# Kernel optimization log

Hardware: AMD Instinct MI355X
Metric: run time of the kernel (lower is better)

The kernel has to match this reference:

```python
import jax, jax.numpy as jnp
import numpy as np

B, N, D, H, L = 16, 1024, 256, 128, 2  # batch, nodes, feat dim, gcn_hidden, n_layers (D == 2*H)


def setup_inputs() -> dict:
    key = jax.random.key(0)
    ks = jax.random.split(key, 16)
    inp = {
        "gcn_input": jax.random.normal(ks[0], (B, N, D), jnp.float32),
        # scale adjacencies by 1/N so aggregated features stay O(1)
        "latent_adj": jax.random.uniform(ks[1], (B, N, N), jnp.float32) / N,
        "dep_adj": jax.random.uniform(ks[2], (B, N, N), jnp.float32) / N,
        # stacked per-layer parameters (leading dim L); layers share shapes since D == 2*H
        "refine_gate": jax.random.normal(ks[3], (L, D, 1), jnp.float32) * 0.02,
        "gate_W_in": jax.random.normal(ks[4], (L, D, 1), jnp.float32) * 0.02,
        "gate_b_in": jnp.zeros((L, 1), jnp.float32),
        "gate_W_out": jax.random.normal(ks[5], (L, D, 1), jnp.float32) * 0.02,
        "gate_b_out": jnp.zeros((L, 1), jnp.float32),
        "fc_in_W": jax.random.normal(ks[6], (L, H, D), jnp.float32) * 0.02,
        "fc_in_b": jnp.zeros((L, H), jnp.float32),
        "fc_out_W": jax.random.normal(ks[7], (L, H, D), jnp.float32) * 0.02,
        "fc_out_b": jnp.zeros((L, H), jnp.float32),
        "ln_g": jnp.ones((L, 2 * H), jnp.float32),
        "ln_b": jnp.zeros((L, 2 * H), jnp.float32),
    }
    return inp


def _gcn_layer(x, latent, dep, rg, Wgi, bgi, Wgo, bgo, Wi, bi, Wo, bo, g, b):
    # refine gate blends dependency and latent adjacency per source node
    gate = jax.nn.sigmoid(x @ rg)  # [B,N,1]
    A_in = gate * dep + (1.0 - gate) * latent  # [B,N,N]
    A_out = gate * jnp.swapaxes(dep, -1, -2) + (1.0 - gate) * jnp.swapaxes(latent, -1, -2)
    Ax_in = A_in @ x   # [B,N,D]
    Ax_out = A_out @ x
    # gcn gates (scalar bias added after the gated product, as in torch)
    Ax_in = Ax_in * jax.nn.sigmoid(Ax_in @ Wgi) + bgi
    Ax_out = Ax_out * jax.nn.sigmoid(Ax_out @ Wgo) + bgo
    # rec_fc(Ax) + rec_fc(x): weight applied to sum, bias counted twice (faithful)
    h_in = (Ax_in + x) @ Wi.T + 2.0 * bi   # [B,N,H]
    h_out = (Ax_out + x) @ Wo.T + 2.0 * bo
    h = jnp.concatenate([h_in, h_out], axis=-1)  # [B,N,2H]
    mu = jnp.mean(h, axis=-1, keepdims=True)
    var = jnp.var(h, axis=-1, keepdims=True)
    h = (h - mu) * jax.lax.rsqrt(var + 1e-5) * g + b
    return jax.nn.gelu(h, approximate=False)


def reference(gcn_input, latent_adj, dep_adj, refine_gate, gate_W_in, gate_b_in,
              gate_W_out, gate_b_out, fc_in_W, fc_in_b, fc_out_W, fc_out_b, ln_g, ln_b):
    x = gcn_input
    for l in range(refine_gate.shape[0]):  # small fixed layer count
        x = _gcn_layer(x, latent_adj, dep_adj, refine_gate[l],
                       gate_W_in[l], gate_b_in[l], gate_W_out[l], gate_b_out[l],
                       fc_in_W[l], fc_in_b[l], fc_out_W[l], fc_out_b[l],
                       ln_g[l], ln_b[l])
    return x
```

## Files before the change

### kernel.cpp

```cpp
#include <hip/hip_runtime.h>
#include <hip/hip_bf16.h>
#include <cstdint>

#define B_ 16
#define N_ 1024
#define D_ 256
#define H_ 128

typedef unsigned short u16;
typedef __attribute__((ext_vector_type(8))) short bf16x8;
typedef __attribute__((ext_vector_type(4))) float f32x4;

__device__ __forceinline__ u16 f2bf(float f) {
    union { float f; uint32_t u; } v; v.f = f;
    return (u16)((v.u + 0x7FFFu + ((v.u >> 16) & 1u)) >> 16);
}
__device__ __forceinline__ float bf2f(u16 h) {
    union { uint32_t u; float f; } v; v.u = ((uint32_t)h) << 16;
    return v.f;
}

typedef __attribute__((address_space(3))) void lds_void;
typedef const __attribute__((address_space(1))) void g_void;

__device__ __forceinline__ void gl_lds16(const void* g, void* l) {
    __builtin_amdgcn_global_load_lds((g_void*)g, (lds_void*)l, 16, 0, 0);
}

__device__ __forceinline__ void vm_wait4() { asm volatile("s_waitcnt vmcnt(4)" ::: "memory"); }
__device__ __forceinline__ void vm_wait3() { asm volatile("s_waitcnt vmcnt(3)" ::: "memory"); }
__device__ __forceinline__ void vm_wait2() { asm volatile("s_waitcnt vmcnt(2)" ::: "memory"); }
__device__ __forceinline__ void vm_wait0() { asm volatile("s_waitcnt vmcnt(0)" ::: "memory"); }
__device__ __forceinline__ void lgkm0()   { asm volatile("s_waitcnt lgkmcnt(0)" ::: "memory"); }
__device__ __forceinline__ void schedb()  { __builtin_amdgcn_sched_barrier(0); }

__global__ __launch_bounds__(256) void k_conv_adj(
    const float* __restrict__ dep, const float* __restrict__ lat,
    u16* __restrict__ depb, u16* __restrict__ latb,
    u16* __restrict__ depTb, u16* __restrict__ latTb)
{
    __shared__ u16 tile[64][64];
    const int bz = blockIdx.z;
    const int b = bz >> 1;
    const float* src = (bz & 1) ? lat : dep;
    u16* dstN = (bz & 1) ? latb : depb;
    u16* dstT = (bz & 1) ? latTb : depTb;
    const int r0 = blockIdx.y * 64, c0 = blockIdx.x * 64;
    const int t = threadIdx.x;
    const int r = t >> 2, cg = (t & 3) * 16;

    const float* srow = src + ((size_t)b * N_ + r0 + r) * N_ + c0 + cg;
    bf16x8 lo, hi;
    {
        const float4 v0 = *(const float4*)(srow);
        const float4 v1 = *(const float4*)(srow + 4);
        const float4 v2 = *(const float4*)(srow + 8);
        const float4 v3 = *(const float4*)(srow + 12);
        lo[0] = (short)f2bf(v0.x); lo[1] = (short)f2bf(v0.y); lo[2] = (short)f2bf(v0.z); lo[3] = (short)f2bf(v0.w);
        lo[4] = (short)f2bf(v1.x); lo[5] = (short)f2bf(v1.y); lo[6] = (short)f2bf(v1.z); lo[7] = (short)f2bf(v1.w);
        hi[0] = (short)f2bf(v2.x); hi[1] = (short)f2bf(v2.y); hi[2] = (short)f2bf(v2.z); hi[3] = (short)f2bf(v2.w);
        hi[4] = (short)f2bf(v3.x); hi[5] = (short)f2bf(v3.y); hi[6] = (short)f2bf(v3.z); hi[7] = (short)f2bf(v3.w);
    }
    u16* nrow = dstN + ((size_t)b * N_ + r0 + r) * N_ + c0 + cg;
    *(bf16x8*)nrow = lo;
    *(bf16x8*)(nrow + 8) = hi;

    const int g0 = (t & 3) * 2;
    const int s = (r & 7) ^ ((r >> 3) & 7);
    *(bf16x8*)(&tile[r][((g0    ) ^ s) * 8]) = lo;
    *(bf16x8*)(&tile[r][((g0 + 1) ^ s) * 8]) = hi;
    __syncthreads();

    const int sc = t >> 2, rg2 = (t & 3) * 16;
    bf16x8 o0, o1;
    #pragma unroll
    for (int i = 0; i < 8; ++i) {
        const int R = rg2 + i;
        const int sR = (R & 7) ^ ((R >> 3) & 7);
        o0[i] = (short)tile[R][(((sc >> 3) ^ sR) * 8) + (sc & 7)];
    }
    #pragma unroll
    for (int i = 0; i < 8; ++i) {
        const int R = rg2 + 8 + i;
        const int sR = (R & 7) ^ ((R >> 3) & 7);
        o1[i] = (short)tile[R][(((sc >> 3) ^ sR) * 8) + (sc & 7)];
    }
    u16* dT = dstT + ((size_t)b * N_ + c0 + sc) * N_ + r0 + rg2;
    *(bf16x8*)dT = o0;
    *(bf16x8*)(dT + 8) = o1;
}

__global__ __launch_bounds__(256) void k_gate_xt(
    const float* __restrict__ x, const float* __restrict__ rg,
    float* __restrict__ gate, u16* __restrict__ xT,
    const float* __restrict__ wi, const float* __restrict__ wo,
    u16* __restrict__ wib, u16* __restrict__ wob)
{
    if (blockIdx.y >= B_) {
        const int i = ((blockIdx.y - B_) * 32 + blockIdx.x) * 256 + threadIdx.x;
        wib[i] = f2bf(wi[i]);
        wob[i] = f2bf(wo[i]);
        return;
    }

    __shared__ u16 lx[D_][36];
    __shared__ float srg[D_];
    const int b = blockIdx.y, n0 = blockIdx.x * 32;
    const int t = threadIdx.x;
    srg[t] = rg[t];
    __syncthreads();

    const int r = t >> 3, cg = t & 7;
    const float* xrow = x + ((size_t)b * N_ + n0 + r) * D_;
    float dot = 0.f;
    #pragma unroll
    for (int u = 0; u < 8; ++u) {
        const int c = cg * 32 + u * 4;
        const float4 v = *(const float4*)(xrow + c);
        lx[c][r] = f2bf(v.x); lx[c + 1][r] = f2bf(v.y);
        lx[c + 2][r] = f2bf(v.z); lx[c + 3][r] = f2bf(v.w);
        dot += v.x * srg[c] + v.y * srg[c + 1] + v.z * srg[c + 2] + v.w * srg[c + 3];
    }
    dot += __shfl_down(dot, 4, 8);
    dot += __shfl_down(dot, 2, 8);
    dot += __shfl_down(dot, 1, 8);
    if (cg == 0) gate[(size_t)b * N_ + n0 + r] = 1.f / (1.f + expf(-dot));
    __syncthreads();

    #pragma unroll
    for (int i = 0; i < 8; ++i) {
        const int unit = i * 256 + t;
        const int d = unit >> 3, nch = (unit & 7) * 4;
        ushort4 wv;
        wv.x = lx[d][nch];     wv.y = lx[d][nch + 1];
        wv.z = lx[d][nch + 2]; wv.w = lx[d][nch + 3];
        *(ushort4*)(xT + ((size_t)b * D_ + d) * N_ + n0 + nch) = wv;
    }
}

__global__ __launch_bounds__(512, 2) void k_gemm_ax(
    const u16* __restrict__ depb, const u16* __restrict__ latb,
    const u16* __restrict__ depTb, const u16* __restrict__ latTb,
    const u16* __restrict__ xT,
    const float* __restrict__ gate,
    const float* __restrict__ Wgi, const float* __restrict__ Wgo,
    const float* __restrict__ bgi, const float* __restrict__ bgo,
    const float* __restrict__ xcur,
    u16* __restrict__ axin, u16* __restrict__ axout)
{
    __shared__ __align__(16) char smem[51712];
    u16* const sb = (u16*)smem;
    float* hbuf = (float*)smem;
    float* psum = (float*)(smem + 49152);
    float* sh_s = (float*)(smem + 51200);

    const int bid = blockIdx.x;
    const int logical = (bid & 7) * 32 + (bid >> 3);
    const int b = logical >> 4;
    const int rem = logical & 15;
    const int z = rem >> 3;
    const int m0 = (rem & 7) * 128;

    const u16* A1 = z ? depTb : depb;
    const u16* A2 = z ? latTb : latb;
    const float* Wg = z ? Wgo : Wgi;
    const float bg0 = z ? bgo[0] : bgi[0];
    u16* outp = z ? axout : axin;

    const int t = threadIdx.x;
    const int lane = t & 63;
    const int w = t >> 6;
    const int wr = w >> 2, wc = w & 3;

    const int arow = t >> 2;
    const int akq = t & 3;
    const float gv = gate[(size_t)b * N_ + m0 + arow];
    const u16* gA1 = A1 + ((size_t)b * N_ + m0 + arow) * N_ + akq * 8;
    const u16* gA2 = A2 + ((size_t)b * N_ + m0 + arow) * N_ + akq * 8;
    const int awoff = arow * 32 + ((akq ^ ((arow >> 1) & 3)) << 3);

    const int rl = lane >> 2;
    const int kk = (((lane & 3) ^ ((lane >> 3) & 3)) << 3);
    const u16* gB0 = xT + ((size_t)b * D_ + (w * 2) * 16 + rl) * N_ + kk;
    const u16* gB1 = xT + ((size_t)b * D_ + (w * 2 + 1) * 16 + rl) * N_ + kk;
    const int boff0 = 4096 + (w * 2) * 512;
    const int boff1 = 4096 + (w * 2 + 1) * 512;

    const int mrow = lane & 15;
    const int hi = lane >> 4;
    const int kg = (((lane >> 4) ^ ((mrow >> 1) & 3)) << 3);

    f32x4 acc[4][4];
    const f32x4 fz = {0.f, 0.f, 0.f, 0.f};
    #pragma unroll
    for (int i = 0; i < 4; ++i)
        #pragma unroll
        for (int j = 0; j < 4; ++j) acc[i][j] = fz;

    bf16x8 rA1x, rA2x, rA1y, rA2y;

    auto blend_store = [&](const bf16x8& a1v, const bf16x8& a2v, u16* dst) {
        bf16x8 bl;
        #pragma unroll
        for (int u = 0; u < 8; ++u) {
            const float f1 = bf2f((u16)a1v[u]);
            const float f2 = bf2f((u16)a2v[u]);
            bl[u] = (short)f2bf(f2 + gv * (f1 - f2));
        }
        *(bf16x8*)dst = bl;
    };

    rA1x = *(const bf16x8*)(gA1);       rA2x = *(const bf16x8*)(gA2);
    blend_store(rA1x, rA2x, sb + awoff);
    rA1x = *(const bf16x8*)(gA1 + 32);  rA2x = *(const bf16x8*)(gA2 + 32);
    gl_lds16(gB0, sb + boff0);          gl_lds16(gB1, sb + boff1);
    blend_store(rA1x, rA2x, sb + 12288 + awoff);
    rA1x = *(const bf16x8*)(gA1 + 64);  rA2x = *(const bf16x8*)(gA2 + 64);
    gl_lds16(gB0 + 32, sb + 12288 + boff0); gl_lds16(gB1 + 32, sb + 12288 + boff1);
    vm_wait2();
    lgkm0();
    schedb(); __builtin_amdgcn_s_barrier(); schedb();

    auto body = [&](int ks, bf16x8& c1, bf16x8& c2, bf16x8& n1, bf16x8& n2) {
        if (ks <= 28) {
            n1 = *(const bf16x8*)(gA1 + (ks + 3) * 32);
            n2 = *(const bf16x8*)(gA2 + (ks + 3) * 32);
        }
        const u16* sA = sb + (ks & 1) * 12288;
        const u16* sBc = sA + 4096;
        bf16x8 a[4], fbv[4];
        #pragma unroll
        for (int mt = 0; mt < 4; ++mt)
            a[mt] = *(const bf16x8*)(sA + (wr * 64 + mt * 16 + mrow) * 32 + kg);
        #pragma unroll
        for (int nt = 0; nt < 4; ++nt)
            fbv[nt] = *(const bf16x8*)(sBc + (wc * 64 + nt * 16 + mrow) * 32 + kg);
        #pragma unroll
        for (int mt = 0; mt < 4; ++mt)
            #pragma unroll
            for (int nt = 0; nt < 4; ++nt)
                acc[mt][nt] = __builtin_amdgcn_mfma_f32_16x16x32_bf16(a[mt], fbv[nt], acc[mt][nt], 0, 0, 0);
        schedb();
        __builtin_amdgcn_s_barrier();
        schedb();
        if (ks <= 29) {
            u16* cb = sb + (ks & 1) * 12288;
            blend_store(c1, c2, cb + awoff);
            gl_lds16(gB0 + (ks + 2) * 32, cb + boff0);
            gl_lds16(gB1 + (ks + 2) * 32, cb + boff1);
        }
        if (ks <= 28) vm_wait4();
        else if (ks == 29) vm_wait2();
        else if (ks == 30) vm_wait0();
        lgkm0();
        schedb();
        __builtin_amdgcn_s_barrier();
        schedb();
    };

    for (int kp = 0; kp < 16; ++kp) {
        body(2 * kp,     rA1x, rA2x, rA1y, rA2y);
        body(2 * kp + 1, rA1y, rA2y, rA1x, rA2x);
    }
    __syncthreads();

    float wgv[4];
    #pragma unroll
    for (int nt = 0; nt < 4; ++nt) wgv[nt] = Wg[wc * 64 + nt * 16 + mrow];
    #pragma unroll
    for (int mt = 0; mt < 4; ++mt) {
        #pragma unroll
        for (int rr = 0; rr < 4; ++rr) {
            float p = acc[mt][0][rr] * wgv[0] + acc[mt][1][rr] * wgv[1]
                    + acc[mt][2][rr] * wgv[2] + acc[mt][3][rr] * wgv[3];
            p += __shfl_xor(p, 1, 16);
            p += __shfl_xor(p, 2, 16);
            p += __shfl_xor(p, 4, 16);
            p += __shfl_xor(p, 8, 16);
            if (mrow == 0) psum[(wr * 64 + mt * 16 + hi * 4 + rr) * 4 + wc] = p;
        }
    }
    __syncthreads();
    if (t < 128) {
        const float d = psum[t * 4] + psum[t * 4 + 1] + psum[t * 4 + 2] + psum[t * 4 + 3];
        sh_s[t] = 1.f / (1.f + expf(-d));
    }
    __syncthreads();

    #pragma unroll
    for (int p = 0; p < 4; ++p) {
        if (wr == (p >> 1)) {
            #pragma unroll
            for (int mtl = 0; mtl < 2; ++mtl) {
                const int mt = (p & 1) * 2 + mtl;
                #pragma unroll
                for (int nt = 0; nt < 4; ++nt) {
                    const int col = wc * 64 + nt * 16 + mrow;
                    #pragma unroll
                    for (int rr = 0; rr < 4; ++rr) {
                        const int hrow = mtl * 16 + hi * 4 + rr;
                        hbuf[hrow * 260 + col] = acc[mt][nt][rr];
                    }
                }
            }
        }
        __syncthreads();
        {
            const int sr = t >> 4;
            const int sc0 = (t & 15) * 16;
            const int grow = p * 32 + sr;
            const float s = sh_s[grow];
            const size_t gb = ((size_t)b * N_ + m0 + grow) * D_ + sc0;
            const float* xr = xcur + gb;
            u16* orow = outp + gb;
            bf16x8 o0, o1;
            #pragma unroll
            for (int u = 0; u < 8; ++u)
                o0[u] = (short)f2bf(hbuf[sr * 260 + sc0 + u] * s + bg0 + xr[u]);
            #pragma unroll
            for (int u = 0; u < 8; ++u)
                o1[u] = (short)f2bf(hbuf[sr * 260 + sc0 + 8 + u] * s + bg0 + xr[8 + u]);
            *(bf16x8*)orow = o0;
            *(bf16x8*)(orow + 8) = o1;
        }
        __syncthreads();
    }
}

template<int FUSE>
__global__ __launch_bounds__(512, 2) void k_fc_ln(
    const u16* __restrict__ axin, const u16* __restrict__ axout,
    const u16* __restrict__ Wib, const u16* __restrict__ Wob,
    const float* __restrict__ bi, const float* __restrict__ bo,
    const float* __restrict__ lg, const float* __restrict__ lb,
    float* __restrict__ outp,
    const float* __restrict__ rgN, float* __restrict__ gateN,
    u16* __restrict__ xTN)
{
    __shared__ __align__(16) char smem[51712];
    u16* const sb = (u16*)smem;
    float* hbuf = (float*)smem;
    float* psum = (float*)(smem + 49152);
    float* sh_mu = (float*)(smem + 51200);
    float* sh_rs = (float*)(smem + 51456);

    const int bid = blockIdx.x;
    const int logical = (bid & 7) * 32 + (bid >> 3);
    const int b = logical >> 4;
    const int m0 = (logical & 15) * 64;

    const int t = threadIdx.x, lane = t & 63, w = t >> 6;
    const int wr = w >> 2, wc = w & 3;
    const int half = wc >> 1;

    const int rl = lane >> 2;
    const int kk = (((lane & 3) ^ ((lane >> 3) & 3)) << 3);

    const u16* gsrc[3];
    int loff[3];
    #pragma unroll
    for (int ci = 0; ci < 3; ++ci) {
        const int c = w * 3 + ci;
        if (c < 4) {
            gsrc[ci] = axin + ((size_t)b * N_ + m0 + c * 16 + rl) * D_ + kk;
            loff[ci] = c * 512;
        } else if (c < 8) {
            gsrc[ci] = axout + ((size_t)b * N_ + m0 + (c - 4) * 16 + rl) * D_ + kk;
            loff[ci] = 2048 + (c - 4) * 512;
        } else {
            const int cw = c - 8;
            const u16* base = (cw < 8) ? (Wib + (size_t)(cw * 16 + rl) * D_)
                                       : (Wob + (size_t)((cw - 8) * 16 + rl) * D_);
            gsrc[ci] = base + kk;
            loff[ci] = 4096 + cw * 512;
        }
    }

    f32x4 acc[2][4];
    const f32x4 fz = {0.f, 0.f, 0.f, 0.f};
    #pragma unroll
    for (int i = 0; i < 2; ++i)
        #pragma unroll
        for (int j = 0; j < 4; ++j) acc[i][j] = fz;

    #pragma unroll
    for (int ci = 0; ci < 3; ++ci) gl_lds16(gsrc[ci], sb + loff[ci]);
    #pragma unroll
    for (int ci = 0; ci < 3; ++ci) gl_lds16(gsrc[ci] + 32, sb + 12288 + loff[ci]);
    vm_wait3();
    lgkm0();
    schedb(); __builtin_amdgcn_s_barrier(); schedb();

    const int mrow = lane & 15;
    const int hi = lane >> 4;
    const int kg = (((lane >> 4) ^ ((mrow >> 1) & 3)) << 3);

    for (int ks = 0; ks < 8; ++ks) {
        const u16* cur = sb + (ks & 1) * 12288;
        const u16* sA = cur + (half ? 2048 : 0);
        const u16* sW = cur + 4096;
        bf16x8 a[2], fbv[4];
        #pragma unroll
        for (int mt = 0; mt < 2; ++mt)
            a[mt] = *(const bf16x8*)(sA + (wr * 32 + mt * 16 + mrow) * 32 + kg);
        #pragma unroll
        for (int nt = 0; nt < 4; ++nt)
            fbv[nt] = *(const bf16x8*)(sW + (wc * 64 + nt * 16 + mrow) * 32 + kg);
        #pragma unroll
        for (int mt = 0; mt < 2; ++mt)
            #pragma unroll
            for (int nt = 0; nt < 4; ++nt)
                acc[mt][nt] = __builtin_amdgcn_mfma_f32_16x16x32_bf16(a[mt], fbv[nt], acc[mt][nt], 0, 0, 0);
        schedb();
        __builtin_amdgcn_s_barrier();
        schedb();
        if (ks <= 5) {
            u16* nb = sb + (ks & 1) * 12288;
            #pragma unroll
            for (int ci = 0; ci < 3; ++ci) gl_lds16(gsrc[ci] + (ks + 2) * 32, nb + loff[ci]);
        }
        if (ks <= 5) vm_wait3();
        else if (ks == 6) vm_wait0();
        lgkm0();
        schedb();
        __builtin_amdgcn_s_barrier();
        schedb();
    }
    __syncthreads();

    float bc[4];
    #pragma unroll
    for (int nt = 0; nt < 4; ++nt) {
        const int colh = wc * 64 + nt * 16 + mrow;
        bc[nt] = 2.f * (colh < 128 ? bi[colh] : bo[colh - 128]);
    }
    #pragma unroll
    for (int mt = 0; mt < 2; ++mt)
        #pragma unroll
        for (int rr = 0; rr < 4; ++rr) {
            const int lrow = wr * 32 + mt * 16 + hi * 4 + rr;
            float s = 0.f, ss = 0.f;
            #pragma unroll
            for (int nt = 0; nt < 4; ++nt) {
                const float v = acc[mt][nt][rr] + bc[nt];
                s += v; ss += v * v;
            }
            s += __shfl_xor(s, 1, 16);  ss += __shfl_xor(ss, 1, 16);
            s += __shfl_xor(s, 2, 16);  ss += __shfl_xor(ss, 2, 16);
            s += __shfl_xor(s, 4, 16);  ss += __shfl_xor(ss, 4, 16);
            s += __shfl_xor(s, 8, 16);  ss += __shfl_xor(ss, 8, 16);
            if (mrow == 0) {
                psum[lrow * 8 + wc * 2] = s;
                psum[lrow * 8 + wc * 2 + 1] = ss;
            }
        }
    __syncthreads();
    if (t < 64) {
        const float s = psum[t * 8] + psum[t * 8 + 2] + psum[t * 8 + 4] + psum[t * 8 + 6];
        const float ss = psum[t * 8 + 1] + psum[t * 8 + 3] + psum[t * 8 + 5] + psum[t * 8 + 7];
        const float mu = s * (1.f / 256.f);
        const float var = ss * (1.f / 256.f) - mu * mu;
        sh_mu[t] = mu;
        sh_rs[t] = rsqrtf(var + 1e-5f);
    }
    __syncthreads();

    #pragma unroll
    for (int p = 0; p < 2; ++p) {
        if (wr == p) {
            #pragma unroll
            for (int mt = 0; mt < 2; ++mt)
                #pragma unroll
                for (int nt = 0; nt < 4; ++nt) {
                    const int col = wc * 64 + nt * 16 + mrow;
                    #pragma unroll
                    for (int rr = 0; rr < 4; ++rr) {
                        const int hrow = mt * 16 + hi * 4 + rr;
                        hbuf[hrow * 260 + col] = acc[mt][nt][rr] + bc[nt];
                    }
                }
        }
        __syncthreads();
        {
            const int sr = t >> 4;
            const int sc0 = (t & 15) * 16;
            const int grow = p * 32 + sr;
            const float mu = sh_mu[grow], rs = sh_rs[grow];
            float* orow = outp + ((size_t)b * N_ + m0 + grow) * D_ + sc0;
            float gdot = 0.f;
            #pragma unroll
            for (int q = 0; q < 4; ++q) {
                const float4 gg = *(const float4*)(lg + sc0 + q * 4);
                const float4 bb = *(const float4*)(lb + sc0 + q * 4);
                float4 o;
                const float v0 = (hbuf[sr * 260 + sc0 + q * 4    ] - mu) * rs * gg.x + bb.x;
                const float v1 = (hbuf[sr * 260 + sc0 + q * 4 + 1] - mu) * rs * gg.y + bb.y;
                const float v2 = (hbuf[sr * 260 + sc0 + q * 4 + 2] - mu) * rs * gg.z + bb.z;
                const float v3 = (hbuf[sr * 260 + sc0 + q * 4 + 3] - mu) * rs * gg.w + bb.w;
                o.x = 0.5f * v0 * (1.f + erff(v0 * 0.70710678118654752f));
                o.y = 0.5f * v1 * (1.f + erff(v1 * 0.70710678118654752f));
                o.z = 0.5f * v2 * (1.f + erff(v2 * 0.70710678118654752f));
                o.w = 0.5f * v3 * (1.f + erff(v3 * 0.70710678118654752f));
                *(float4*)(orow + q * 4) = o;
                if (FUSE) {
                    hbuf[sr * 260 + sc0 + q * 4    ] = o.x;
                    hbuf[sr * 260 + sc0 + q * 4 + 1] = o.y;
                    hbuf[sr * 260 + sc0 + q * 4 + 2] = o.z;
                    hbuf[sr * 260 + sc0 + q * 4 + 3] = o.w;
                    const float4 rv = *(const float4*)(rgN + sc0 + q * 4);
                    gdot += o.x * rv.x + o.y * rv.y + o.z * rv.z + o.w * rv.w;
                }
            }
            if (FUSE) {
                gdot += __shfl_xor(gdot, 1, 16);
                gdot += __shfl_xor(gdot, 2, 16);
                gdot += __shfl_xor(gdot, 4, 16);
                gdot += __shfl_xor(gdot, 8, 16);
                if ((t & 15) == 0)
                    gateN[(size_t)b * N_ + m0 + grow] = 1.f / (1.f + expf(-gdot));
            }
        }
        __syncthreads();
        if (FUSE) {
            const int d = t >> 1;
            const int nh = (t & 1) * 16;
            bf16x8 y0, y1;
            #pragma unroll
            for (int i = 0; i < 8; ++i)
                y0[i] = (short)f2bf(hbuf[(nh + i) * 260 + d]);
            #pragma unroll
            for (int i = 0; i < 8; ++i)
                y1[i] = (short)f2bf(hbuf[(nh + 8 + i) * 260 + d]);
            u16* xrow = xTN + ((size_t)b * D_ + d) * N_ + m0 + p * 32 + nh;
            *(bf16x8*)xrow = y0;
            *(bf16x8*)(xrow + 8) = y1;
            __syncthreads();
        }
    }
}

extern "C" void kernel_launch(void* const* d_in, const int* in_sizes, int n_in,
                              void* d_out, int out_size, void* d_ws, size_t ws_size,
                              hipStream_t stream)
{
    (void)in_sizes; (void)n_in; (void)out_size; (void)ws_size;

    const float* x0  = (const float*)d_in[0];
    const float* lat = (const float*)d_in[1];
    const float* dep = (const float*)d_in[2];
    const float* rg  = (const float*)d_in[3];
    const float* Wgi = (const float*)d_in[4];
    const float* bgi = (const float*)d_in[5];
    const float* Wgo = (const float*)d_in[6];
    const float* bgo = (const float*)d_in[7];
    const float* fiW = (const float*)d_in[8];
    const float* fib = (const float*)d_in[9];
    const float* foW = (const float*)d_in[10];
    const float* fob = (const float*)d_in[11];
    const float* lng = (const float*)d_in[12];
    const float* lnb = (const float*)d_in[13];

    char* ws = (char*)d_ws;
    size_t off = 0;
    auto alloc = [&](size_t bytes) {
        char* p = ws + off;
        off += (bytes + 255) & ~(size_t)255;
        return p;
    };
    u16* depb  = (u16*)alloc(2ull * B_ * N_ * N_);
    u16* latb  = (u16*)alloc(2ull * B_ * N_ * N_);
    u16* depTb = (u16*)alloc(2ull * B_ * N_ * N_);
    u16* latTb = (u16*)alloc(2ull * B_ * N_ * N_);
    u16* xT    = (u16*)alloc(2ull * B_ * D_ * N_);
    u16* axin  = (u16*)alloc(2ull * B_ * N_ * D_);
    u16* axout = (u16*)alloc(2ull * B_ * N_ * D_);
    float* gate = (float*)alloc(4ull * B_ * N_);
    float* xbuf = (float*)alloc(4ull * B_ * N_ * D_);
    u16* Wib = (u16*)alloc(2ull * 2 * H_ * D_);
    u16* Wob = (u16*)alloc(2ull * 2 * H_ * D_);

    k_conv_adj<<<dim3(16, 16, 32), 256, 0, stream>>>(dep, lat, depb, latb, depTb, latTb);

    k_gate_xt<<<dim3(32, B_ + 8), 256, 0, stream>>>(
        x0, rg, gate, xT, fiW, foW, Wib, Wob);

    k_gemm_ax<<<dim3(256), 512, 0, stream>>>(
        depb, latb, depTb, latTb, xT, gate,
        Wgi, Wgo, bgi, bgo, x0, axin, axout);
    k_fc_ln<1><<<dim3(256), 512, 0, stream>>>(
        axin, axout, Wib, Wob, fib, fob, lng, lnb,
        xbuf, rg + D_, gate, xT);

    k_gemm_ax<<<dim3(256), 512, 0, stream>>>(
        depb, latb, depTb, latTb, xT, gate,
        Wgi + D_, Wgo + D_, bgi + 1, bgo + 1, xbuf, axin, axout);
    k_fc_ln<0><<<dim3(256), 512, 0, stream>>>(
        axin, axout, Wib + (size_t)H_ * D_, Wob + (size_t)H_ * D_,
        fib + H_, fob + H_, lng + 2 * H_, lnb + 2 * H_,
        (float*)d_out, nullptr, nullptr, nullptr);
}
```

Before: 320.8 us.

## Double K tile to 64 per stage in adjacency GEMM with wider swizzle

Widens the K step of the blended-adjacency × x GEMM from 32 to 64. This halves the number of pipeline stages and barrier pairs, and each stage now issues two MFMA sub-steps. LDS buffers grow to about 100KB and use a new 8-way XOR swizzle, and the vmcnt waits are adjusted for the larger number of loads in flight. The larger LDS footprint may cut the two-blocks-per-CU occupancy the launch bounds target, and more A registers are held per thread.

```diff
diff --git a/kernel.cpp b/kernel.cpp
--- a/kernel.cpp
+++ b/kernel.cpp
@@ -27,9 +27,9 @@
     __builtin_amdgcn_global_load_lds((g_void*)g, (lds_void*)l, 16, 0, 0);
 }
 
+__device__ __forceinline__ void vm_wait8() { asm volatile("s_waitcnt vmcnt(8)" ::: "memory"); }
 __device__ __forceinline__ void vm_wait4() { asm volatile("s_waitcnt vmcnt(4)" ::: "memory"); }
 __device__ __forceinline__ void vm_wait3() { asm volatile("s_waitcnt vmcnt(3)" ::: "memory"); }
-__device__ __forceinline__ void vm_wait2() { asm volatile("s_waitcnt vmcnt(2)" ::: "memory"); }
 __device__ __forceinline__ void vm_wait0() { asm volatile("s_waitcnt vmcnt(0)" ::: "memory"); }
 __device__ __forceinline__ void lgkm0()   { asm volatile("s_waitcnt lgkmcnt(0)" ::: "memory"); }
 __device__ __forceinline__ void schedb()  { __builtin_amdgcn_sched_barrier(0); }
@@ -148,11 +148,11 @@
     const float* __restrict__ xcur,
     u16* __restrict__ axin, u16* __restrict__ axout)
 {
-    __shared__ __align__(16) char smem[51712];
+    __shared__ __align__(16) char smem[100864];
     u16* const sb = (u16*)smem;
     float* hbuf = (float*)smem;
-    float* psum = (float*)(smem + 49152);
-    float* sh_s = (float*)(smem + 51200);
+    float* psum = (float*)(smem + 98304);
+    float* sh_s = (float*)(smem + 100352);
 
     const int bid = blockIdx.x;
     const int logical = (bid & 7) * 32 + (bid >> 3);
@@ -173,22 +173,24 @@
     const int wr = w >> 2, wc = w & 3;
 
     const int arow = t >> 2;
-    const int akq = t & 3;
+    const int aq = t & 3;
     const float gv = gate[(size_t)b * N_ + m0 + arow];
-    const u16* gA1 = A1 + ((size_t)b * N_ + m0 + arow) * N_ + akq * 8;
-    const u16* gA2 = A2 + ((size_t)b * N_ + m0 + arow) * N_ + akq * 8;
-    const int awoff = arow * 32 + ((akq ^ ((arow >> 1) & 3)) << 3);
-
-    const int rl = lane >> 2;
-    const int kk = (((lane & 3) ^ ((lane >> 3) & 3)) << 3);
-    const u16* gB0 = xT + ((size_t)b * D_ + (w * 2) * 16 + rl) * N_ + kk;
-    const u16* gB1 = xT + ((size_t)b * D_ + (w * 2 + 1) * 16 + rl) * N_ + kk;
-    const int boff0 = 4096 + (w * 2) * 512;
-    const int boff1 = 4096 + (w * 2 + 1) * 512;
+    const u16* gA1 = A1 + ((size_t)b * N_ + m0 + arow) * N_ + aq * 8;
+    const u16* gA2 = A2 + ((size_t)b * N_ + m0 + arow) * N_ + aq * 8;
+    const int awoff = arow * 64 + ((aq ^ (arow & 7)) << 3);
+
+    const int kksrc = (((lane & 7) ^ ((lane >> 3) & 7)) << 3);
+    const u16* gB[4];
+    int boff[4];
+    #pragma unroll
+    for (int j = 0; j < 4; ++j) {
+        const int ch = w * 4 + j;
+        gB[j] = xT + ((size_t)b * D_ + ch * 8 + (lane >> 3)) * N_ + kksrc;
+        boff[j] = 8192 + ch * 512;
+    }
 
     const int mrow = lane & 15;
     const int hi = lane >> 4;
-    const int kg = (((lane >> 4) ^ ((mrow >> 1) & 3)) << 3);
 
     f32x4 acc[4][4];
     const f32x4 fz = {0.f, 0.f, 0.f, 0.f};
@@ -197,9 +199,16 @@
         #pragma unroll
         for (int j = 0; j < 4; ++j) acc[i][j] = fz;
 
-    bf16x8 rA1x, rA2x, rA1y, rA2y;
-
-    auto blend_store = [&](const bf16x8& a1v, const bf16x8& a2v, u16* dst) {
+    struct S { bf16x8 a1l, a1h, a2l, a2h; };
+    S sx, sy;
+
+    auto loadA = [&](S& s, int ks) {
+        s.a1l = *(const bf16x8*)(gA1 + ks * 64);
+        s.a1h = *(const bf16x8*)(gA1 + ks * 64 + 32);
+        s.a2l = *(const bf16x8*)(gA2 + ks * 64);
+        s.a2h = *(const bf16x8*)(gA2 + ks * 64 + 32);
+    };
+    auto blend8 = [&](const bf16x8& a1v, const bf16x8& a2v) {
         bf16x8 bl;
         #pragma unroll
         for (int u = 0; u < 8; ++u) {
@@ -207,60 +216,70 @@
             const float f2 = bf2f((u16)a2v[u]);
             bl[u] = (short)f2bf(f2 + gv * (f1 - f2));
         }
-        *(bf16x8*)dst = bl;
+        return bl;
     };
-
-    rA1x = *(const bf16x8*)(gA1);       rA2x = *(const bf16x8*)(gA2);
-    blend_store(rA1x, rA2x, sb + awoff);
-    rA1x = *(const bf16x8*)(gA1 + 32);  rA2x = *(const bf16x8*)(gA2 + 32);
-    gl_lds16(gB0, sb + boff0);          gl_lds16(gB1, sb + boff1);
-    blend_store(rA1x, rA2x, sb + 12288 + awoff);
-    rA1x = *(const bf16x8*)(gA1 + 64);  rA2x = *(const bf16x8*)(gA2 + 64);
-    gl_lds16(gB0 + 32, sb + 12288 + boff0); gl_lds16(gB1 + 32, sb + 12288 + boff1);
-    vm_wait2();
+    auto blend_store = [&](const S& s, u16* cb) {
+        *(bf16x8*)(cb + awoff) = blend8(s.a1l, s.a2l);
+        *(bf16x8*)(cb + (awoff ^ 32)) = blend8(s.a1h, s.a2h);
+    };
+
+    loadA(sx, 0); blend_store(sx, sb);
+    loadA(sx, 1); blend_store(sx, sb + 24576);
+    #pragma unroll
+    for (int j = 0; j < 4; ++j) gl_lds16(gB[j], sb + boff[j]);
+    loadA(sx, 2);
+    #pragma unroll
+    for (int j = 0; j < 4; ++j) gl_lds16(gB[j] + 64, sb + 24576 + boff[j]);
+    vm_wait8();
     lgkm0();
     schedb(); __builtin_amdgcn_s_barrier(); schedb();
 
-    auto body = [&](int ks, bf16x8& c1, bf16x8& c2, bf16x8& n1, bf16x8& n2) {
-        if (ks <= 28) {
-            n1 = *(const bf16x8*)(gA1 + (ks + 3) * 32);
-            n2 = *(const bf16x8*)(gA2 + (ks + 3) * 32);
-        }
-        const u16* sA = sb + (ks & 1) * 12288;
-        const u16* sBc = sA + 4096;
-        bf16x8 a[4], fbv[4];
-        #pragma unroll
-        for (int mt = 0; mt < 4; ++mt)
-            a[mt] = *(const bf16x8*)(sA + (wr * 64 + mt * 16 + mrow) * 32 + kg);
-        #pragma unroll
-        for (int nt = 0; nt < 4; ++nt)
-            fbv[nt] = *(const bf16x8*)(sBc + (wc * 64 + nt * 16 + mrow) * 32 + kg);
-        #pragma unroll
-        for (int mt = 0; mt < 4; ++mt)
-            #pragma unroll
-            for (int nt = 0; nt < 4; ++nt)
-                acc[mt][nt] = __builtin_amdgcn_mfma_f32_16x16x32_bf16(a[mt], fbv[nt], acc[mt][nt], 0, 0, 0);
+    auto body = [&](int ks, S& cS, S& nS) {
+        if (ks <= 12) loadA(nS, ks + 3);
+        const u16* sA = sb + (ks & 1) * 24576;
+        const u16* sBc = sA + 8192;
+        #pragma unroll
+        for (int kh = 0; kh < 2; ++kh) {
+            bf16x8 a[4], fbv[4];
+            #pragma unroll
+            for (int mt = 0; mt < 4; ++mt) {
+                const int row = wr * 64 + mt * 16 + mrow;
+                const int slot = (kh * 4 + hi) ^ (mrow & 7);
+                a[mt] = *(const bf16x8*)(sA + row * 64 + slot * 8);
+            }
+            #pragma unroll
+            for (int nt = 0; nt < 4; ++nt) {
+                const int row = wc * 64 + nt * 16 + mrow;
+                const int slot = (kh * 4 + hi) ^ (mrow & 7);
+                fbv[nt] = *(const bf16x8*)(sBc + row * 64 + slot * 8);
+            }
+            #pragma unroll
+            for (int mt = 0; mt < 4; ++mt)
+                #pragma unroll
+                for (int nt = 0; nt < 4; ++nt)
+                    acc[mt][nt] = __builtin_amdgcn_mfma_f32_16x16x32_bf16(a[mt], fbv[nt], acc[mt][nt], 0, 0, 0);
+        }
         schedb();
         __builtin_amdgcn_s_barrier();
         schedb();
-        if (ks <= 29) {
-            u16* cb = sb + (ks & 1) * 12288;
-            blend_store(c1, c2, cb + awoff);
-            gl_lds16(gB0 + (ks + 2) * 32, cb + boff0);
-            gl_lds16(gB1 + (ks + 2) * 32, cb + boff1);
-        }
-        if (ks <= 28) vm_wait4();
-        else if (ks == 29) vm_wait2();
-        else if (ks == 30) vm_wait0();
+        if (ks <= 13) {
+            u16* cb = sb + (ks & 1) * 24576;
+            blend_store(cS, cb);
+            #pragma unroll
+            for (int j = 0; j < 4; ++j) gl_lds16(gB[j] + (ks + 2) * 64, cb + boff[j]);
+        }
+        if (ks <= 12) vm_wait8();
+        else if (ks == 13) vm_wait4();
+        else if (ks == 14) vm_wait0();
         lgkm0();
         schedb();
         __builtin_amdgcn_s_barrier();
         schedb();
     };
 
-    for (int kp = 0; kp < 16; ++kp) {
-        body(2 * kp,     rA1x, rA2x, rA1y, rA2y);
-        body(2 * kp + 1, rA1y, rA2y, rA1x, rA2x);
+    for (int kp = 0; kp < 8; ++kp) {
+        body(2 * kp,     sx, sy);
+        body(2 * kp + 1, sy, sx);
     }
     __syncthreads();
 
```

New measurement: 321.8 us. Within noise of the previous version (+0.3%).
